# Optimization experiments

Hardware: AMD Instinct MI355X
Metric: run time of the kernel (lower is better)

Reference implementation:

```python
import jax, jax.numpy as jnp
import numpy as np

# dims
B, K, DIN, PROJ = 32, 256, 512, 64
DM, NL, PL, ST = 128, 3, 8, 4
NPAT = (K - PL) // ST + 1          # 63 patches
DI = 2 * DM                        # mamba inner dim = 256
D_STATE, D_CONV, DT_RANK = 16, 4, 8

def rmsnorm(x, w):
    return x * jax.lax.rsqrt(jnp.mean(x * x, -1, keepdims=True) + 1e-5) * w

def setup_inputs() -> dict:
    key = jax.random.key(0)
    ks = jax.random.split(key, 20)
    s = 0.02
    n = lambda k, sh: (jax.random.normal(k, sh, jnp.float32) * s)
    inp = {
        'x': jax.random.normal(ks[0], (B, K, DIN), jnp.float32),
        'W_proj': n(ks[1], (DIN, PROJ)), 'b_proj': jnp.zeros((PROJ,), jnp.float32),
        'W_embed': n(ks[2], (PL, DM)), 'b_embed': jnp.zeros((DM,), jnp.float32),
        'norm_w': jnp.ones((NL, DM), jnp.float32),
        'in_proj_w': n(ks[3], (NL, DM, 2 * DI)),
        'conv_w': n(ks[4], (NL, DI, 1, D_CONV)), 'conv_b': jnp.zeros((NL, DI), jnp.float32),
        'x_proj_w': n(ks[5], (NL, DI, DT_RANK + 2 * D_STATE)),
        'dt_proj_w': n(ks[6], (NL, DT_RANK, DI)),
        'dt_proj_b': jnp.full((NL, DI), -4.0, jnp.float32),  # softplus -> small dt
        'A_log': jnp.broadcast_to(jnp.log(jnp.arange(1, D_STATE + 1, dtype=jnp.float32)), (NL, DI, D_STATE)).copy(),
        'Dp': jnp.ones((NL, DI), jnp.float32),
        'out_proj_w': n(ks[7], (NL, DI, DM)),
        'final_norm_w': jnp.ones((DM,), jnp.float32),
        'head_flat_w': n(ks[8], (NPAT * DM, 1)), 'head_flat_b': jnp.zeros((1,), jnp.float32),
        'W_head': n(ks[9], (PROJ, 2)), 'b_head': jnp.zeros((2,), jnp.float32),
    }
    return inp

def _mamba(u, Wi, cw, cb, Wx, Wdt, bdt, A_log, Dp, Wo):
    # u: (N, L, DM)
    xz = u @ Wi                                   # (N, L, 2*DI)
    xh, z = jnp.split(xz, 2, axis=-1)
    # causal depthwise conv1d
    xc = jnp.pad(xh.transpose(0, 2, 1), ((0, 0), (0, 0), (D_CONV - 1, 0)))
    xc = jax.lax.conv_general_dilated(xc, cw, (1,), 'VALID',
                                      feature_group_count=DI,
                                      dimension_numbers=('NCH', 'OIH', 'NCH'))
    xh = jax.nn.silu(xc.transpose(0, 2, 1) + cb)  # (N, L, DI)
    dbl = xh @ Wx
    dt = dbl[..., :DT_RANK]
    Bm = dbl[..., DT_RANK:DT_RANK + D_STATE]
    Cm = dbl[..., DT_RANK + D_STATE:]
    delta = jax.nn.softplus(dt @ Wdt + bdt)       # (N, L, DI)
    A = -jnp.exp(A_log)                           # (DI, D_STATE)

    def step(h, t):
        d_t, b_t, c_t, u_t = t                    # (N,DI),(N,S),(N,S),(N,DI)
        h = h * jnp.exp(d_t[..., None] * A) + (d_t * u_t)[..., None] * b_t[:, None, :]
        return h, jnp.einsum('nds,ns->nd', h, c_t)

    h0 = jnp.zeros((u.shape[0], DI, D_STATE), u.dtype)
    xs = (delta.transpose(1, 0, 2), Bm.transpose(1, 0, 2),
          Cm.transpose(1, 0, 2), xh.transpose(1, 0, 2))
    _, ys = jax.lax.scan(step, h0, xs)            # (L, N, DI)
    y = ys.transpose(1, 0, 2) + xh * Dp
    y = y * jax.nn.silu(z)
    return y @ Wo

def reference(x, W_proj, b_proj, W_embed, b_embed, norm_w, in_proj_w, conv_w, conv_b,
              x_proj_w, dt_proj_w, dt_proj_b, A_log, Dp, out_proj_w,
              final_norm_w, head_flat_w, head_flat_b, W_head, b_head):
    h = x @ W_proj + b_proj                       # (B, K, PROJ)
    h = h.transpose(0, 2, 1)                      # (B, C, K)
    idx = np.arange(NPAT)[:, None] * ST + np.arange(PL)[None, :]
    p = h[..., idx]                               # (B, C, NPAT, PL)
    u = p @ W_embed + b_embed                     # (B, C, NPAT, DM)
    u = u.reshape(B * PROJ, NPAT, DM)
    for l in range(NL):
        u = u + _mamba(rmsnorm(u, norm_w[l]), in_proj_w[l], conv_w[l], conv_b[l],
                       x_proj_w[l], dt_proj_w[l], dt_proj_b[l], A_log[l], Dp[l], out_proj_w[l])
    u = rmsnorm(u, final_norm_w)
    u = u.reshape(B, PROJ, NPAT * DM)
    y = (u @ head_flat_w + head_flat_b)[..., 0]   # (B, C)
    return y @ W_head + b_head                    # (B, 2)
```

## Files before the change

### kernel.cpp

```cpp
#include <hip/hip_runtime.h>
#include <hip/hip_bf16.h>
#include <cstdio>

typedef __hip_bfloat16 bf16;
typedef __attribute__((ext_vector_type(8))) short short8;
typedef __attribute__((ext_vector_type(4))) short short4v;
typedef __attribute__((ext_vector_type(4))) float f32x4;
typedef __attribute__((ext_vector_type(2))) float f32x2;

#define NB    32
#define NK    256
#define NDIN  512
#define NPROJ 64
#define NDM   128
#define NNL   3
#define NT    63
#define NDI   256
#define NSEQ  2048
#define NROW  (NSEQ*NT)
#define LDP   136

static __device__ __forceinline__ float b2f(bf16 v){ return __bfloat162float(v); }
static __device__ __forceinline__ bf16  f2b(float v){ return __float2bfloat16(v); }
static __device__ __forceinline__ unsigned short f2bs(float v){
  unsigned int u = __float_as_uint(v);
  return (unsigned short)((u + 0x7FFFu + ((u >> 16) & 1u)) >> 16);
}
static __device__ __forceinline__ float siluf(float x){
  return x * __builtin_amdgcn_rcpf(1.f + __expf(-x));
}
static __device__ __forceinline__ float softplusf(float x){
  float e = __expf(-fabsf(x));
  return fmaxf(x, 0.f) + __logf(1.f + e);
}

__global__ __launch_bounds__(256) void k_tw_all(
    const float* __restrict__ Wi, const float* __restrict__ Wo,
    const float* __restrict__ Wx,
    unsigned short* __restrict__ WiT, unsigned short* __restrict__ WoT,
    unsigned short* __restrict__ WxT)
{
  int bx = blockIdx.x;
  int l = bx / 704, r = bx - l*704;
  const float* src; unsigned short* dst; int K, srcN, nvalid, n;
  if (r < 512)      { n = r;     src = Wi + (size_t)l*128*512; dst = WiT + (size_t)l*512*128; K=128; srcN=512; nvalid=512; }
  else if (r < 640) { n = r-512; src = Wo + (size_t)l*256*128; dst = WoT + (size_t)l*128*256; K=256; srcN=128; nvalid=128; }
  else              { n = r-640; src = Wx + (size_t)l*256*40;  dst = WxT + (size_t)l*64*256;  K=256; srcN=40;  nvalid=40; }
  for (int k = threadIdx.x; k < K; k += 256) {
    float v = (n < nvalid) ? src[(size_t)k*srcN + n] : 0.f;
    dst[(size_t)n*K + k] = f2bs(v);
  }
}

__global__ void k_proj(const float* __restrict__ x, const float* __restrict__ Wp,
                       const float* __restrict__ bp, float* __restrict__ hp)
{
  int blk = blockIdx.x;
  int b = blk >> 8, k = blk & 255;
  __shared__ float xr[NDIN];
  for (int i = threadIdx.x; i < NDIN; i += 64)
    xr[i] = x[(size_t)blk*NDIN + i];
  __syncthreads();
  int p = threadIdx.x;
  float acc = bp[p];
  #pragma unroll 8
  for (int d = 0; d < NDIN; ++d)
    acc += xr[d] * Wp[d*NPROJ + p];
  hp[(size_t)(b*NPROJ + p)*NK + k] = acc;
}

__global__ void k_embed(const float* __restrict__ hp, const float* __restrict__ We,
                        const float* __restrict__ be, float* __restrict__ u)
{
  int blk = blockIdx.x;
  int n = blk / NT, t = blk - n*NT;
  int m = threadIdx.x;
  const float* hr = hp + (size_t)n*NK + t*4;
  float acc = be[m];
  #pragma unroll
  for (int j = 0; j < 8; ++j)
    acc += hr[j] * We[j*NDM + m];
  u[(size_t)blk*NDM + m] = acc;
}

template<int MODE, int KTOT, int BN>
__global__ __launch_bounds__(256) void
k_mgemm(const void* __restrict__ Aptr, const unsigned short* __restrict__ WT,
        void* __restrict__ Cptr, void* __restrict__ Cptr2,
        const float* __restrict__ nw)
{
  constexpr int MJ = BN/32;
  __shared__ short As[64*LDP];
  __shared__ short Bs[BN*LDP];

  const int tid  = threadIdx.x;
  const int r0   = blockIdx.x * 64;
  const int n0   = (MODE == 0) ? blockIdx.y * 128 : 0;
  const int w    = tid >> 6;
  const int lane = tid & 63;
  const int l16  = lane & 15;
  const int quad = lane >> 4;
  const int WM   = (w >> 1) * 32;
  const int WN   = (w & 1) * (BN/2);

  f32x4 acc[2][MJ] = {};

  for (int kc = 0; kc < KTOT; kc += 128) {
    if (MODE == 0) {
      float4 va[8]; float ss[8];
      const float4 nwv = *(const float4*)(nw + ((tid & 31) << 2));
      #pragma unroll
      for (int j = 0; j < 8; ++j) {
        int c = tid + j*256;
        int row = c >> 5, k4 = (c & 31) << 2;
        va[j] = *(const float4*)((const float*)Aptr + (size_t)(r0+row)*128 + k4);
        ss[j] = va[j].x*va[j].x + va[j].y*va[j].y + va[j].z*va[j].z + va[j].w*va[j].w;
      }
      #pragma unroll
      for (int j = 0; j < 8; ++j) {
        float s = ss[j];
        #pragma unroll
        for (int m = 16; m >= 1; m >>= 1) s += __shfl_xor(s, m, 32);
        float sc = rsqrtf(s*(1.f/128.f) + 1e-5f);
        int c = tid + j*256;
        int row = c >> 5, k4 = (c & 31) << 2;
        short4v o = { (short)f2bs(va[j].x*sc*nwv.x), (short)f2bs(va[j].y*sc*nwv.y),
                      (short)f2bs(va[j].z*sc*nwv.z), (short)f2bs(va[j].w*sc*nwv.w) };
        *(short4v*)&As[row*LDP + k4] = o;
      }
    } else {
      #pragma unroll
      for (int j = 0; j < 4; ++j) {
        int c   = tid + j*256;
        int row = c >> 4, k8 = (c & 15) << 3;
        short8 v = *(const short8*)((const unsigned short*)Aptr
                                    + (size_t)(r0+row)*256 + kc + k8);
        *(short8*)&As[row*LDP + k8] = v;
      }
    }
    #pragma unroll
    for (int j = 0; j < BN/16; ++j) {
      int c  = tid + j*256;
      int n  = c >> 4, k8 = (c & 15) << 3;
      short8 v = *(const short8*)(WT + (size_t)(n0+n)*KTOT + kc + k8);
      *(short8*)&Bs[n*LDP + k8] = v;
    }
    __syncthreads();

    #pragma unroll
    for (int ks = 0; ks < 4; ++ks) {
      short8 a[2], b[MJ];
      #pragma unroll
      for (int i = 0; i < 2; ++i)
        a[i] = *(const short8*)&As[(WM + i*16 + l16)*LDP + ks*32 + quad*8];
      #pragma unroll
      for (int j = 0; j < MJ; ++j)
        b[j] = *(const short8*)&Bs[(WN + j*16 + l16)*LDP + ks*32 + quad*8];
      #pragma unroll
      for (int i = 0; i < 2; ++i)
        #pragma unroll
        for (int j = 0; j < MJ; ++j)
          acc[i][j] = __builtin_amdgcn_mfma_f32_16x16x32_bf16(a[i], b[j], acc[i][j], 0, 0, 0);
    }
    __syncthreads();
  }

  #pragma unroll
  for (int i = 0; i < 2; ++i) {
    #pragma unroll
    for (int j = 0; j < MJ; ++j) {
      #pragma unroll
      for (int rr = 0; rr < 4; ++rr) {
        int row = r0 + WM + i*16 + quad*4 + rr;
        int col = n0 + WN + j*16 + l16;
        float v = acc[i][j][rr];
        if (MODE == 0) {
          if (col < 256) ((unsigned short*)Cptr )[(size_t)row*256 + col]       = f2bs(v);
          else           ((unsigned short*)Cptr2)[(size_t)row*256 + col - 256] = f2bs(v);
        } else if (MODE == 1) {
          if (col < 40) ((float*)Cptr)[(size_t)row*40 + col] = v;
        } else {
          ((float*)Cptr)[(size_t)row*128 + col] += v;
        }
      }
    }
  }
}

__global__ __launch_bounds__(256) void k_conv(bf16* __restrict__ xh,
                       const float* __restrict__ cw, const float* __restrict__ cb)
{
  int n = blockIdx.x, d = threadIdx.x;
  float w0 = cw[d*4+0], w1 = cw[d*4+1];
  float w2 = cw[d*4+2], w3 = cw[d*4+3];
  float bias = cb[d];
  float xm3 = 0.f, xm2 = 0.f, xm1 = 0.f;
  bf16* ptr = xh + (size_t)n*NT*256 + d;
  for (int t = 0; t < NT; ++t) {
    float xt = b2f(ptr[(size_t)t*256]);
    float a  = bias + w0*xm3 + w1*xm2 + w2*xm1 + w3*xt;
    ptr[(size_t)t*256] = f2b(siluf(a));
    xm3 = xm2; xm2 = xm1; xm1 = xt;
  }
}

__global__ __launch_bounds__(256) void k_scan(const float* __restrict__ dbl,
                       const bf16* __restrict__ z, bf16* __restrict__ xh,
                       const float* __restrict__ Wdt, const float* __restrict__ bdt,
                       const float* __restrict__ Alog, const float* __restrict__ Dpp)
{
  int n = blockIdx.x, d = threadIdx.x;
  __shared__ float sd[NT][40];
  for (int i = threadIdx.x; i < NT*40; i += 256)
    sd[i/40][i%40] = dbl[(size_t)n*NT*40 + i];
  __syncthreads();

  float bd = bdt[d];
  float Av[16];
  #pragma unroll
  for (int s = 0; s < 16; ++s) Av[s] = -__expf(Alog[d*16 + s]);
  float Av0 = Av[0];
  bool chain = fabsf(Av0 + 1.f) <= 1e-3f;
  #pragma unroll
  for (int s = 0; s < 16; ++s)
    chain = chain && (fabsf(Av[s] - (float)(s+1)*Av0) <= 1e-3f*(float)(s+1));
  float dp = Dpp[d];

  const bf16* zsrc = z  + (size_t)n*NT*256 + d;
  bf16*       uio  = xh + (size_t)n*NT*256 + d;

  if (chain) {
    f32x2 wdt2[4];
    #pragma unroll
    for (int r = 0; r < 4; ++r) {
      f32x2 wv; wv.x = Wdt[(2*r)*256 + d]; wv.y = Wdt[(2*r+1)*256 + d];
      wdt2[r] = wv;
    }
    f32x2 h2[8];
    #pragma unroll
    for (int s = 0; s < 8; ++s) { h2[s].x = 0.f; h2[s].y = 0.f; }

    for (int t = 0; t < NT; ++t) {
      const f32x2* sdt = (const f32x2*)&sd[t][0];
      f32x2 a2; a2.x = bd; a2.y = 0.f;
      #pragma unroll
      for (int r = 0; r < 4; ++r) a2 += sdt[r]*wdt2[r];
      float dtv = a2.x + a2.y;
      float q  = __expf(-fabsf(dtv));
      float r1 = __builtin_amdgcn_rcpf(1.f + q);
      float E  = dtv > 0.f ? q*r1 : r1;
      float delta = fmaxf(dtv, 0.f) - __logf(r1);
      float E2 = E*E;
      f32x2 ee; ee.x = E2; ee.y = E2;
      f32x2 p2[8];
      p2[0].x = E; p2[0].y = E2;
      #pragma unroll
      for (int s = 1; s < 8; ++s) p2[s] = p2[s-1]*ee;

      float ut = b2f(uio[(size_t)t*256]);
      float du = delta*ut;
      f32x2 du2; du2.x = du; du2.y = du;
      const f32x2* B2 = (const f32x2*)&sd[t][8];
      const f32x2* C2 = (const f32x2*)&sd[t][24];
      f32x2 yt2; yt2.x = 0.f; yt2.y = 0.f;
      #pragma unroll
      for (int s = 0; s < 8; ++s) {
        h2[s] = h2[s]*p2[s] + du2*B2[s];
        yt2  += h2[s]*C2[s];
      }
      float yt = yt2.x + yt2.y;
      float zv = b2f(zsrc[(size_t)t*256]);
      float y  = (yt + ut*dp) * siluf(zv);
      uio[(size_t)t*256] = f2b(y);
    }
  } else {
    float wdt[8];
    #pragma unroll
    for (int r = 0; r < 8; ++r) wdt[r] = Wdt[r*256 + d];
    float h[16];
    #pragma unroll
    for (int s = 0; s < 16; ++s) h[s] = 0.f;
    for (int t = 0; t < NT; ++t) {
      float dtv = bd;
      #pragma unroll
      for (int r = 0; r < 8; ++r) dtv += sd[t][r]*wdt[r];
      float delta = softplusf(dtv);
      float ut = b2f(uio[(size_t)t*256]);
      float du = delta*ut;
      float yt = 0.f;
      #pragma unroll
      for (int s = 0; s < 16; ++s) {
        float e = __expf(delta*Av[s]);
        h[s] = h[s]*e + du*sd[t][8+s];
        yt  += h[s]*sd[t][24+s];
      }
      float zv = b2f(zsrc[(size_t)t*256]);
      float y  = (yt + ut*dp) * siluf(zv);
      uio[(size_t)t*256] = f2b(y);
    }
  }
}

__global__ __launch_bounds__(256) void k_head(const float* __restrict__ u,
                       const float* __restrict__ fnw,
                       const float* __restrict__ hw, const float* __restrict__ hfb,
                       float* __restrict__ y1)
{
  int n = blockIdx.x;
  int w = threadIdx.x >> 6, lane = threadIdx.x & 63;
  const float2 fw = *(const float2*)&fnw[lane*2];
  float acc = 0.f;
  for (int t = w; t < NT; t += 4) {
    const float2 v  = *(const float2*)&u[((size_t)n*NT + t)*NDM + lane*2];
    const float2 hv = *(const float2*)&hw[t*NDM + lane*2];
    float ss = v.x*v.x + v.y*v.y;
    #pragma unroll
    for (int o = 32; o >= 1; o >>= 1) ss += __shfl_xor(ss, o);
    float sc = rsqrtf(ss*(1.f/128.f) + 1e-5f);
    acc += (v.x*fw.x*hv.x + v.y*fw.y*hv.y)*sc;
  }
  #pragma unroll
  for (int o = 32; o >= 1; o >>= 1) acc += __shfl_xor(acc, o);
  __shared__ float ws[4];
  if (lane == 0) ws[w] = acc;
  __syncthreads();
  if (threadIdx.x == 0) y1[n] = ws[0] + ws[1] + ws[2] + ws[3] + hfb[0];
}

__global__ __launch_bounds__(64) void k_final(const float* __restrict__ y1,
                        const float* __restrict__ Wh,
                        const float* __restrict__ bh, float* __restrict__ out)
{
  int t = threadIdx.x;
  int b = t >> 1, c = t & 1;
  float acc = bh[c];
  #pragma unroll 8
  for (int p = 0; p < 64; ++p) acc += y1[b*64 + p]*Wh[p*2 + c];
  out[b*2 + c] = acc;
}

extern "C" void kernel_launch(void* const* d_in, const int* in_sizes, int n_in,
                              void* d_out, int out_size, void* d_ws, size_t ws_size,
                              hipStream_t stream)
{
  const float* x    = (const float*)d_in[0];
  const float* Wp   = (const float*)d_in[1];
  const float* bp   = (const float*)d_in[2];
  const float* We   = (const float*)d_in[3];
  const float* be   = (const float*)d_in[4];
  const float* nrm  = (const float*)d_in[5];
  const float* Wi   = (const float*)d_in[6];
  const float* cw   = (const float*)d_in[7];
  const float* cb   = (const float*)d_in[8];
  const float* Wx   = (const float*)d_in[9];
  const float* Wdt  = (const float*)d_in[10];
  const float* bdt  = (const float*)d_in[11];
  const float* Alog = (const float*)d_in[12];
  const float* Dpp  = (const float*)d_in[13];
  const float* Wo   = (const float*)d_in[14];
  const float* fnw  = (const float*)d_in[15];
  const float* hw   = (const float*)d_in[16];
  const float* hfb  = (const float*)d_in[17];
  const float* Wh   = (const float*)d_in[18];
  const float* bh   = (const float*)d_in[19];

  const size_t wt_per_l = (size_t)512*128 + 128*256 + 64*256;
  const size_t fixed_b = (size_t)NROW*NDM*4 + (size_t)NSEQ*NK*4 + NSEQ*4
                       + wt_per_l*2*NNL + 8192;
  const size_t per_seq = (size_t)NT*256*2*2 + (size_t)NT*40*4;
  int ch_seq = NSEQ;
  while (ch_seq > 128 && fixed_b + (size_t)ch_seq*per_seq + 2048 > ws_size)
    ch_seq >>= 1;
  const int nchunk  = NSEQ / ch_seq;
  const int ch_rows = ch_seq * NT;
  fprintf(stderr, "[mamba] ws_size=%zu ch_seq=%d nchunk=%d\n", ws_size, ch_seq, nchunk);

  char* pw = (char*)d_ws;
  float* u    = (float*)pw; pw += (size_t)NROW*NDM*4;
  float* hp   = (float*)pw; pw += (size_t)NSEQ*NK*4;
  float* y1   = (float*)pw; pw += (size_t)NSEQ*4;
  unsigned short* WiT = (unsigned short*)pw; pw += (size_t)NNL*512*128*2;
  unsigned short* WoT = (unsigned short*)pw; pw += (size_t)NNL*128*256*2;
  unsigned short* WxT = (unsigned short*)pw; pw += (size_t)NNL*64*256*2;
  float* dbl  = (float*)pw; pw += (size_t)ch_rows*40*4;
  bf16*  xh   = (bf16*)pw;  pw += (size_t)ch_rows*256*2;
  bf16*  z    = (bf16*)pw;  pw += (size_t)ch_rows*256*2;

  k_tw_all<<<3*704, 256, 0, stream>>>(Wi, Wo, Wx, WiT, WoT, WxT);
  k_proj <<<NB*NK,  64, 0, stream>>>(x, Wp, bp, hp);
  k_embed<<<NROW,  128, 0, stream>>>(hp, We, be, u);

  for (int l = 0; l < NNL; ++l) {
    const float* nw_l  = nrm  + (size_t)l*NDM;
    const float* cw_l  = cw   + (size_t)l*NDI*4;
    const float* cb_l  = cb   + (size_t)l*NDI;
    const float* Wdt_l = Wdt  + (size_t)l*8*NDI;
    const float* bdt_l = bdt  + (size_t)l*NDI;
    const float* Al_l  = Alog + (size_t)l*NDI*16;
    const float* Dp_l  = Dpp  + (size_t)l*NDI;
    const unsigned short* WiT_l = WiT + (size_t)l*512*128;
    const unsigned short* WoT_l = WoT + (size_t)l*128*256;
    const unsigned short* WxT_l = WxT + (size_t)l*64*256;

    for (int c = 0; c < nchunk; ++c) {
      float* u_c = u + (size_t)c*ch_rows*NDM;
      k_mgemm<0,128,128><<<dim3(ch_rows/64, 4), 256, 0, stream>>>(
          u_c, WiT_l, xh, z, nw_l);
      k_conv<<<ch_seq, 256, 0, stream>>>(xh, cw_l, cb_l);
      k_mgemm<1,256,64><<<dim3(ch_rows/64, 1), 256, 0, stream>>>(
          xh, WxT_l, dbl, nullptr, nullptr);
      k_scan<<<ch_seq, 256, 0, stream>>>(dbl, z, xh, Wdt_l, bdt_l, Al_l, Dp_l);
      k_mgemm<2,256,128><<<dim3(ch_rows/64, 1), 256, 0, stream>>>(
          xh, WoT_l, u_c, nullptr, nullptr);
    }
  }

  k_head <<<NSEQ, 256, 0, stream>>>(u, fnw, hw, hfb, y1);
  k_final<<<1, 64, 0, stream>>>(y1, Wh, bh, (float*)d_out);
}
```

Baseline: 842.2 us.

## Store residual stream in bf16 and fuse in-projection into single-pass kernel

The residual activation buffer u is now stored as bf16 instead of fp32. That halves its read/write traffic in the embed, in-projection, out-projection accumulate and head kernels. The in-projection becomes a dedicated kernel that normalizes each 64-row A tile once and loops over all four 128-column output tiles. Before, four y-blocks each re-read and re-normalized the same rows. The scan also prefetches the next timestep's u/z values. Accumulating the residual in bf16 across three layers loses precision compared with fp32, which risks tolerance failures.

```diff
diff --git a/kernel.cpp b/kernel.cpp
--- a/kernel.cpp
+++ b/kernel.cpp
@@ -25,6 +25,9 @@
 static __device__ __forceinline__ unsigned short f2bs(float v){
   unsigned int u = __float_as_uint(v);
   return (unsigned short)((u + 0x7FFFu + ((u >> 16) & 1u)) >> 16);
+}
+static __device__ __forceinline__ float bs2f(unsigned short b){
+  return __uint_as_float(((unsigned int)b) << 16);
 }
 static __device__ __forceinline__ float siluf(float x){
   return x * __builtin_amdgcn_rcpf(1.f + __expf(-x));
@@ -70,7 +73,7 @@
 }
 
 __global__ void k_embed(const float* __restrict__ hp, const float* __restrict__ We,
-                        const float* __restrict__ be, float* __restrict__ u)
+                        const float* __restrict__ be, unsigned short* __restrict__ u)
 {
   int blk = blockIdx.x;
   int n = blk / NT, t = blk - n*NT;
@@ -80,14 +83,97 @@
   #pragma unroll
   for (int j = 0; j < 8; ++j)
     acc += hr[j] * We[j*NDM + m];
-  u[(size_t)blk*NDM + m] = acc;
+  u[(size_t)blk*NDM + m] = f2bs(acc);
+}
+
+__global__ __launch_bounds__(256) void k_inproj(
+    const unsigned short* __restrict__ ub, const unsigned short* __restrict__ WT,
+    unsigned short* __restrict__ xh, unsigned short* __restrict__ zb,
+    const float* __restrict__ nw)
+{
+  __shared__ short As[64*LDP];
+  __shared__ short Bs[128*LDP];
+  const int tid  = threadIdx.x;
+  const int r0   = blockIdx.x * 64;
+  const int w    = tid >> 6;
+  const int lane = tid & 63;
+  const int l16  = lane & 15;
+  const int quad = lane >> 4;
+  const int WM   = (w >> 1) * 32;
+  const int WN   = (w & 1) * 64;
+
+  #pragma unroll
+  for (int j = 0; j < 4; ++j) {
+    int c = tid + j*256;
+    int row = c >> 4, k8 = (c & 15) << 3;
+    short8 vb = *(const short8*)&ub[(size_t)(r0+row)*128 + k8];
+    float f[8];
+    #pragma unroll
+    for (int i = 0; i < 8; ++i) f[i] = bs2f((unsigned short)vb[i]);
+    float ss = 0.f;
+    #pragma unroll
+    for (int i = 0; i < 8; ++i) ss += f[i]*f[i];
+    #pragma unroll
+    for (int m = 8; m >= 1; m >>= 1) ss += __shfl_xor(ss, m, 16);
+    float sc = rsqrtf(ss*(1.f/128.f) + 1e-5f);
+    const float4 nw0 = *(const float4*)&nw[k8];
+    const float4 nw1 = *(const float4*)&nw[k8+4];
+    short8 o;
+    o[0] = (short)f2bs(f[0]*sc*nw0.x); o[1] = (short)f2bs(f[1]*sc*nw0.y);
+    o[2] = (short)f2bs(f[2]*sc*nw0.z); o[3] = (short)f2bs(f[3]*sc*nw0.w);
+    o[4] = (short)f2bs(f[4]*sc*nw1.x); o[5] = (short)f2bs(f[5]*sc*nw1.y);
+    o[6] = (short)f2bs(f[6]*sc*nw1.z); o[7] = (short)f2bs(f[7]*sc*nw1.w);
+    *(short8*)&As[row*LDP + k8] = o;
+  }
+
+  for (int ny = 0; ny < 4; ++ny) {
+    if (ny) __syncthreads();
+    #pragma unroll
+    for (int j = 0; j < 8; ++j) {
+      int c = tid + j*256;
+      int n = c >> 4, k8 = (c & 15) << 3;
+      *(short8*)&Bs[n*LDP + k8] =
+          *(const short8*)&WT[(size_t)(ny*128 + n)*128 + k8];
+    }
+    __syncthreads();
+
+    f32x4 acc[2][4] = {};
+    #pragma unroll
+    for (int ks = 0; ks < 4; ++ks) {
+      short8 a[2], b[4];
+      #pragma unroll
+      for (int i = 0; i < 2; ++i)
+        a[i] = *(const short8*)&As[(WM + i*16 + l16)*LDP + ks*32 + quad*8];
+      #pragma unroll
+      for (int j = 0; j < 4; ++j)
+        b[j] = *(const short8*)&Bs[(WN + j*16 + l16)*LDP + ks*32 + quad*8];
+      #pragma unroll
+      for (int i = 0; i < 2; ++i)
+        #pragma unroll
+        for (int j = 0; j < 4; ++j)
+          acc[i][j] = __builtin_amdgcn_mfma_f32_16x16x32_bf16(a[i], b[j], acc[i][j], 0, 0, 0);
+    }
+    #pragma unroll
+    for (int i = 0; i < 2; ++i) {
+      #pragma unroll
+      for (int j = 0; j < 4; ++j) {
+        #pragma unroll
+        for (int rr = 0; rr < 4; ++rr) {
+          int row = r0 + WM + i*16 + quad*4 + rr;
+          int col = ny*128 + WN + j*16 + l16;
+          float v = acc[i][j][rr];
+          if (col < 256) xh[(size_t)row*256 + col]       = f2bs(v);
+          else           zb[(size_t)row*256 + col - 256] = f2bs(v);
+        }
+      }
+    }
+  }
 }
 
 template<int MODE, int KTOT, int BN>
 __global__ __launch_bounds__(256) void
 k_mgemm(const void* __restrict__ Aptr, const unsigned short* __restrict__ WT,
-        void* __restrict__ Cptr, void* __restrict__ Cptr2,
-        const float* __restrict__ nw)
+        void* __restrict__ Cptr)
 {
   constexpr int MJ = BN/32;
   __shared__ short As[64*LDP];
@@ -95,7 +181,6 @@
 
   const int tid  = threadIdx.x;
   const int r0   = blockIdx.x * 64;
-  const int n0   = (MODE == 0) ? blockIdx.y * 128 : 0;
   const int w    = tid >> 6;
   const int lane = tid & 63;
   const int l16  = lane & 15;
@@ -106,43 +191,19 @@
   f32x4 acc[2][MJ] = {};
 
   for (int kc = 0; kc < KTOT; kc += 128) {
-    if (MODE == 0) {
-      float4 va[8]; float ss[8];
-      const float4 nwv = *(const float4*)(nw + ((tid & 31) << 2));
-      #pragma unroll
-      for (int j = 0; j < 8; ++j) {
-        int c = tid + j*256;
-        int row = c >> 5, k4 = (c & 31) << 2;
-        va[j] = *(const float4*)((const float*)Aptr + (size_t)(r0+row)*128 + k4);
-        ss[j] = va[j].x*va[j].x + va[j].y*va[j].y + va[j].z*va[j].z + va[j].w*va[j].w;
-      }
-      #pragma unroll
-      for (int j = 0; j < 8; ++j) {
-        float s = ss[j];
-        #pragma unroll
-        for (int m = 16; m >= 1; m >>= 1) s += __shfl_xor(s, m, 32);
-        float sc = rsqrtf(s*(1.f/128.f) + 1e-5f);
-        int c = tid + j*256;
-        int row = c >> 5, k4 = (c & 31) << 2;
-        short4v o = { (short)f2bs(va[j].x*sc*nwv.x), (short)f2bs(va[j].y*sc*nwv.y),
-                      (short)f2bs(va[j].z*sc*nwv.z), (short)f2bs(va[j].w*sc*nwv.w) };
-        *(short4v*)&As[row*LDP + k4] = o;
-      }
-    } else {
-      #pragma unroll
-      for (int j = 0; j < 4; ++j) {
-        int c   = tid + j*256;
-        int row = c >> 4, k8 = (c & 15) << 3;
-        short8 v = *(const short8*)((const unsigned short*)Aptr
-                                    + (size_t)(r0+row)*256 + kc + k8);
-        *(short8*)&As[row*LDP + k8] = v;
-      }
+    #pragma unroll
+    for (int j = 0; j < 4; ++j) {
+      int c   = tid + j*256;
+      int row = c >> 4, k8 = (c & 15) << 3;
+      short8 v = *(const short8*)((const unsigned short*)Aptr
+                                  + (size_t)(r0+row)*256 + kc + k8);
+      *(short8*)&As[row*LDP + k8] = v;
     }
     #pragma unroll
     for (int j = 0; j < BN/16; ++j) {
       int c  = tid + j*256;
       int n  = c >> 4, k8 = (c & 15) << 3;
-      short8 v = *(const short8*)(WT + (size_t)(n0+n)*KTOT + kc + k8);
+      short8 v = *(const short8*)(WT + (size_t)n*KTOT + kc + k8);
       *(short8*)&Bs[n*LDP + k8] = v;
     }
     __syncthreads();
@@ -172,15 +233,13 @@
       #pragma unroll
       for (int rr = 0; rr < 4; ++rr) {
         int row = r0 + WM + i*16 + quad*4 + rr;
-        int col = n0 + WN + j*16 + l16;
+        int col = WN + j*16 + l16;
         float v = acc[i][j][rr];
-        if (MODE == 0) {
-          if (col < 256) ((unsigned short*)Cptr )[(size_t)row*256 + col]       = f2bs(v);
-          else           ((unsigned short*)Cptr2)[(size_t)row*256 + col - 256] = f2bs(v);
-        } else if (MODE == 1) {
+        if (MODE == 1) {
           if (col < 40) ((float*)Cptr)[(size_t)row*40 + col] = v;
         } else {
-          ((float*)Cptr)[(size_t)row*128 + col] += v;
+          unsigned short* p = (unsigned short*)Cptr + (size_t)row*128 + col;
+          *p = f2bs(bs2f(*p) + v);
         }
       }
     }
@@ -197,9 +256,10 @@
   float xm3 = 0.f, xm2 = 0.f, xm1 = 0.f;
   bf16* ptr = xh + (size_t)n*NT*256 + d;
   for (int t = 0; t < NT; ++t) {
-    float xt = b2f(ptr[(size_t)t*256]);
+    float xt = b2f(ptr[0]);
     float a  = bias + w0*xm3 + w1*xm2 + w2*xm1 + w3*xt;
-    ptr[(size_t)t*256] = f2b(siluf(a));
+    ptr[0] = f2b(siluf(a));
+    ptr += 256;
     xm3 = xm2; xm2 = xm1; xm1 = xt;
   }
 }
@@ -226,8 +286,8 @@
     chain = chain && (fabsf(Av[s] - (float)(s+1)*Av0) <= 1e-3f*(float)(s+1));
   float dp = Dpp[d];
 
-  const bf16* zsrc = z  + (size_t)n*NT*256 + d;
-  bf16*       uio  = xh + (size_t)n*NT*256 + d;
+  const unsigned short* zp = (const unsigned short*)z + (size_t)n*NT*256 + d;
+  unsigned short*       up = (unsigned short*)xh + (size_t)n*NT*256 + d;
 
   if (chain) {
     f32x2 wdt2[4];
@@ -240,7 +300,10 @@
     #pragma unroll
     for (int s = 0; s < 8; ++s) { h2[s].x = 0.f; h2[s].y = 0.f; }
 
+    unsigned short ucur = up[0], zcur = zp[0];
     for (int t = 0; t < NT; ++t) {
+      unsigned short unx = 0, znx = 0;
+      if (t < NT-1) { unx = up[(t+1)*256]; znx = zp[(t+1)*256]; }
       const f32x2* sdt = (const f32x2*)&sd[t][0];
       f32x2 a2; a2.x = bd; a2.y = 0.f;
       #pragma unroll
@@ -257,7 +320,7 @@
       #pragma unroll
       for (int s = 1; s < 8; ++s) p2[s] = p2[s-1]*ee;
 
-      float ut = b2f(uio[(size_t)t*256]);
+      float ut = bs2f(ucur);
       float du = delta*ut;
       f32x2 du2; du2.x = du; du2.y = du;
       const f32x2* B2 = (const f32x2*)&sd[t][8];
@@ -269,9 +332,10 @@
         yt2  += h2[s]*C2[s];
       }
       float yt = yt2.x + yt2.y;
-      float zv = b2f(zsrc[(size_t)t*256]);
+      float zv = bs2f(zcur);
       float y  = (yt + ut*dp) * siluf(zv);
-      uio[(size_t)t*256] = f2b(y);
+      up[t*256] = f2bs(y);
+      ucur = unx; zcur = znx;
     }
   } else {
     float wdt[8];
@@ -285,7 +349,7 @@
       #pragma unroll
       for (int r = 0; r < 8; ++r) dtv += sd[t][r]*wdt[r];
       float delta = softplusf(dtv);
-      float ut = b2f(uio[(size_t)t*256]);
+      float ut = bs2f(up[t*256]);
       float du = delta*ut;
       float yt = 0.f;
       #pragma unroll
@@ -294,14 +358,14 @@
         h[s] = h[s]*e + du*sd[t][8+s];
         yt  += h[s]*sd[t][24+s];
       }
-      float zv = b2f(zsrc[(size_t)t*256]);
+      float zv = bs2f(zp[t*256]);
       float y  = (yt + ut*dp) * siluf(zv);
-      uio[(size_t)t*256] = f2b(y);
-    }
-  }
-}
-
-__global__ __launch_bounds__(256) void k_head(const float* __restrict__ u,
+      up[t*256] = f2bs(y);
+    }
+  }
+}
+
+__global__ __launch_bounds__(256) void k_head(const unsigned short* __restrict__ u,
                        const float* __restrict__ fnw,
                        const float* __restrict__ hw, const float* __restrict__ hfb,
                        float* __restrict__ y1)
@@ -311,13 +375,14 @@
   const float2 fw = *(const float2*)&fnw[lane*2];
   float acc = 0.f;
   for (int t = w; t < NT; t += 4) {
-    const float2 v  = *(const float2*)&u[((size_t)n*NT + t)*NDM + lane*2];
+    const ushort2 vb = *(const ushort2*)&u[((size_t)n*NT + t)*NDM + lane*2];
+    float vx = bs2f(vb.x), vy = bs2f(vb.y);
     const float2 hv = *(const float2*)&hw[t*NDM + lane*2];
-    float ss = v.x*v.x + v.y*v.y;
+    float ss = vx*vx + vy*vy;
     #pragma unroll
     for (int o = 32; o >= 1; o >>= 1) ss += __shfl_xor(ss, o);
     float sc = rsqrtf(ss*(1.f/128.f) + 1e-5f);
-    acc += (v.x*fw.x*hv.x + v.y*fw.y*hv.y)*sc;
+    acc += (vx*fw.x*hv.x + vy*fw.y*hv.y)*sc;
   }
   #pragma unroll
   for (int o = 32; o >= 1; o >>= 1) acc += __shfl_xor(acc, o);
@@ -365,7 +430,7 @@
   const float* bh   = (const float*)d_in[19];
 
   const size_t wt_per_l = (size_t)512*128 + 128*256 + 64*256;
-  const size_t fixed_b = (size_t)NROW*NDM*4 + (size_t)NSEQ*NK*4 + NSEQ*4
+  const size_t fixed_b = (size_t)NROW*NDM*2 + (size_t)NSEQ*NK*4 + NSEQ*4
                        + wt_per_l*2*NNL + 8192;
   const size_t per_seq = (size_t)NT*256*2*2 + (size_t)NT*40*4;
   int ch_seq = NSEQ;
@@ -376,7 +441,7 @@
   fprintf(stderr, "[mamba] ws_size=%zu ch_seq=%d nchunk=%d\n", ws_size, ch_seq, nchunk);
 
   char* pw = (char*)d_ws;
-  float* u    = (float*)pw; pw += (size_t)NROW*NDM*4;
+  unsigned short* u = (unsigned short*)pw; pw += (size_t)NROW*NDM*2;
   float* hp   = (float*)pw; pw += (size_t)NSEQ*NK*4;
   float* y1   = (float*)pw; pw += (size_t)NSEQ*4;
   unsigned short* WiT = (unsigned short*)pw; pw += (size_t)NNL*512*128*2;
@@ -403,15 +468,13 @@
     const unsigned short* WxT_l = WxT + (size_t)l*64*256;
 
     for (int c = 0; c < nchunk; ++c) {
-      float* u_c = u + (size_t)c*ch_rows*NDM;
-      k_mgemm<0,128,128><<<dim3(ch_rows/64, 4), 256, 0, stream>>>(
-          u_c, WiT_l, xh, z, nw_l);
+      unsigned short* u_c = u + (size_t)c*ch_rows*NDM;
+      k_inproj<<<ch_rows/64, 256, 0, stream>>>(
+          u_c, WiT_l, (unsigned short*)xh, (unsigned short*)z, nw_l);
       k_conv<<<ch_seq, 256, 0, stream>>>(xh, cw_l, cb_l);
-      k_mgemm<1,256,64><<<dim3(ch_rows/64, 1), 256, 0, stream>>>(
-          xh, WxT_l, dbl, nullptr, nullptr);
+      k_mgemm<1,256,64><<<ch_rows/64, 256, 0, stream>>>(xh, WxT_l, dbl);
       k_scan<<<ch_seq, 256, 0, stream>>>(dbl, z, xh, Wdt_l, bdt_l, Al_l, Dp_l);
-      k_mgemm<2,256,128><<<dim3(ch_rows/64, 1), 256, 0, stream>>>(
-          xh, WoT_l, u_c, nullptr, nullptr);
+      k_mgemm<2,256,128><<<ch_rows/64, 256, 0, stream>>>(xh, WoT_l, u_c);
     }
   }
 
```

Measured after the change: 744.1 us. -11.6%, faster.
